# Kernel optimization log

Hardware: AMD Instinct MI355X
Metric: run time of the kernel (lower is better)

Reference implementation:

```python
import jax, jax.numpy as jnp
import numpy as np


def _box_filter(img):
    # img: [B,1,H,W]; 5x5 uniform kernel, padding=4 -> output [B,1,H+4,W+4]
    k = jnp.full((1, 1, 5, 5), 1.0 / 25.0, dtype=img.dtype)
    return jax.lax.conv_general_dilated(
        img, k, window_strides=(1, 1), padding=((4, 4), (4, 4)),
        dimension_numbers=('NCHW', 'OIHW', 'NCHW'))


def setup_inputs() -> dict:
    key = jax.random.key(0)
    k1, k2 = jax.random.split(key)
    x = jax.random.normal(k1, (64, 1, 512, 512), dtype=jnp.float32)
    y = jax.random.normal(k2, (64, 1, 512, 512), dtype=jnp.float32)
    return {"x": x, "y": y}


def reference(x, y):
    diff = _box_filter(x) - _box_filter(y)
    # faithful to torch.mean(torch.sqrt(diff * diff)) (== mean(|diff|))
    return jnp.mean(jnp.sqrt(diff * diff))
```

## Files before the change

### kernel.cpp

```cpp
#include <hip/hip_runtime.h>


#define IMG_W 512
#define IMG_H 512
#define OUT_W 516
#define OUT_H 516
#define R     8
#define SPI   65
#define NT    256
#define WAVES (NT / 64)
#define NSTRIPS (64 * SPI)
#define NBLK  (NSTRIPS / WAVES)
#define NPART 64
#define DEPTH 4

__global__ __launch_bounds__(NT, 3) void box_loss_kernel(
    const float* __restrict__ x, const float* __restrict__ y,
    float* __restrict__ partial)
{
    const int t    = threadIdx.x;
    const int lane = t & 63;
    const int wid  = t >> 6;

    const int bid  = blockIdx.x;
    const int swz  = (bid & 7) * (NBLK / 8) + (bid >> 3);

    const int strip = swz * WAVES + wid;
    const int b  = strip / SPI;
    const int s  = strip - b * SPI;
    const int i0 = s * R;
    const int c0 = lane * 8;

    const float* xb = x + (size_t)b * (IMG_W * IMG_H) + c0;
    const float* yb = y + (size_t)b * (IMG_W * IMG_H) + c0;

    float4 sxa[DEPTH], sxc[DEPTH], sya[DEPTH], syc[DEPTH];

    auto issue = [&](int p, int r) {
        const int rc = min(max(r, 0), IMG_H - 1);
        const float* xr = xb + (size_t)rc * IMG_W;
        const float* yr = yb + (size_t)rc * IMG_W;
        sxa[p] = *(const float4*)(xr);
        sxc[p] = *(const float4*)(xr + 4);
        sya[p] = *(const float4*)(yr);
        syc[p] = *(const float4*)(yr + 4);
    };

    #pragma unroll
    for (int p = 0; p < DEPTH; ++p) issue(p, i0 - 4 + p);

    float ring[5][8];
    float v[8];
    #pragma unroll
    for (int j = 0; j < 8; ++j) { v[j] = 0.f; ring[4][j] = 0.f; }

    float acc = 0.f;

    #pragma unroll
    for (int k = 0; k < R + 4; ++k) {
        const int r = i0 - 4 + k;
        const int p = k % DEPTH;
        const float m = (r >= 0 && r < IMG_H) ? 1.f : 0.f;

        float d[8];
        d[0] = (sxa[p].x - sya[p].x) * m; d[1] = (sxa[p].y - sya[p].y) * m;
        d[2] = (sxa[p].z - sya[p].z) * m; d[3] = (sxa[p].w - sya[p].w) * m;
        d[4] = (sxc[p].x - syc[p].x) * m; d[5] = (sxc[p].y - syc[p].y) * m;
        d[6] = (sxc[p].z - syc[p].z) * m; d[7] = (sxc[p].w - syc[p].w) * m;

        if (k + DEPTH < R + 4) issue(p, r + DEPTH);

        if (k < 4) {
            #pragma unroll
            for (int j = 0; j < 8; ++j) { ring[k][j] = d[j]; v[j] += d[j]; }
        } else {
            const int i = i0 + (k - 4);
            const int slot = k % 5;
            #pragma unroll
            for (int j = 0; j < 8; ++j) {
                v[j] += d[j] - ring[slot][j];
                ring[slot][j] = d[j];
            }

            float h0 = __shfl_up(v[4], 1, 64);
            float h1 = __shfl_up(v[5], 1, 64);
            float h2 = __shfl_up(v[6], 1, 64);
            float h3 = __shfl_up(v[7], 1, 64);
            if (lane == 0) { h0 = 0.f; h1 = 0.f; h2 = 0.f; h3 = 0.f; }

            const float s0 = h0 + h1 + h2 + h3 + v[0];
            const float s1 = s0 + v[1] - h0;
            const float s2 = s1 + v[2] - h1;
            const float s3 = s2 + v[3] - h2;
            const float s4 = s3 + v[4] - h3;
            const float s5 = s4 + v[5] - v[0];
            const float s6 = s5 + v[6] - v[1];
            const float s7 = s6 + v[7] - v[2];

            const float rowmask = (i < OUT_H) ? 1.f : 0.f;
            acc += rowmask * (fabsf(s0) + fabsf(s1) + fabsf(s2) + fabsf(s3)
                            + fabsf(s4) + fabsf(s5) + fabsf(s6) + fabsf(s7));

            const float em = (lane == 63) ? rowmask : 0.f;
            const float e0 = v[4] + v[5] + v[6] + v[7];
            const float e1 = v[5] + v[6] + v[7];
            const float e2 = v[6] + v[7];
            const float e3 = v[7];
            acc += em * (fabsf(e0) + fabsf(e1) + fabsf(e2) + fabsf(e3));
        }
    }

    #pragma unroll
    for (int off = 32; off > 0; off >>= 1)
        acc += __shfl_down(acc, off, 64);
    if (lane == 0)
        atomicAdd(partial + (strip & (NPART - 1)), acc);
}

__global__ void finalize_kernel(const float* __restrict__ partial,
                                float* __restrict__ out)
{
    float s = 0.f;
    #pragma unroll
    for (int k = 0; k < NPART; ++k) s += partial[k];
    out[0] = s * (1.0f / (25.0f * 64.0f * 516.0f * 516.0f));
}

extern "C" void kernel_launch(void* const* d_in, const int* in_sizes, int n_in,
                              void* d_out, int out_size, void* d_ws, size_t ws_size,
                              hipStream_t stream) {
    const float* x = (const float*)d_in[0];
    const float* y = (const float*)d_in[1];
    float* out = (float*)d_out;
    float* ws  = (float*)d_ws;

    hipMemsetAsync(ws, 0, NPART * sizeof(float), stream);

    dim3 grid(NBLK);
    box_loss_kernel<<<grid, NT, 0, stream>>>(x, y, ws);
    finalize_kernel<<<1, 1, 0, stream>>>(ws, out);
}
```

Before: 173.2 us.

## Load rows in sched-barrier-fenced chunks and lengthen strips to nine rows

```diff
diff --git a/kernel.cpp b/kernel.cpp
--- a/kernel.cpp
+++ b/kernel.cpp
@@ -5,16 +5,34 @@
 #define IMG_H 512
 #define OUT_W 516
 #define OUT_H 516
-#define R     8
-#define SPI   65
+#define R     9
+#define SPI   58
 #define NT    256
 #define WAVES (NT / 64)
 #define NSTRIPS (64 * SPI)
 #define NBLK  (NSTRIPS / WAVES)
 #define NPART 64
-#define DEPTH 4
+#define NROWS 13
 
-__global__ __launch_bounds__(NT, 3) void box_loss_kernel(
+typedef float v4f __attribute__((ext_vector_type(4)));
+
+#define LOADCHUNK(base, nr)                                               \
+    __builtin_amdgcn_sched_barrier(0);                                    \
+    _Pragma("unroll")                                                     \
+    for (int q = 0; q < (nr); ++q) {                                      \
+        const int rc = min(max(i0 - 4 + (base) + q, 0), IMG_H - 1);       \
+        const float* xr = xb + (size_t)rc * IMG_W;                        \
+        xa[q] = *(const v4f*)(xr); xc[q] = *(const v4f*)(xr + 4);         \
+    }                                                                     \
+    _Pragma("unroll")                                                     \
+    for (int q = 0; q < (nr); ++q) {                                      \
+        const int rc = min(max(i0 - 4 + (base) + q, 0), IMG_H - 1);       \
+        const float* yr = yb + (size_t)rc * IMG_W;                        \
+        ya[q] = *(const v4f*)(yr); yc[q] = *(const v4f*)(yr + 4);         \
+    }                                                                     \
+    __builtin_amdgcn_sched_barrier(0);
+
+__global__ __launch_bounds__(NT, 2) void box_loss_kernel(
     const float* __restrict__ x, const float* __restrict__ y,
     float* __restrict__ partial)
 {
@@ -34,20 +52,7 @@
     const float* xb = x + (size_t)b * (IMG_W * IMG_H) + c0;
     const float* yb = y + (size_t)b * (IMG_W * IMG_H) + c0;
 
-    float4 sxa[DEPTH], sxc[DEPTH], sya[DEPTH], syc[DEPTH];
-
-    auto issue = [&](int p, int r) {
-        const int rc = min(max(r, 0), IMG_H - 1);
-        const float* xr = xb + (size_t)rc * IMG_W;
-        const float* yr = yb + (size_t)rc * IMG_W;
-        sxa[p] = *(const float4*)(xr);
-        sxc[p] = *(const float4*)(xr + 4);
-        sya[p] = *(const float4*)(yr);
-        syc[p] = *(const float4*)(yr + 4);
-    };
-
-    #pragma unroll
-    for (int p = 0; p < DEPTH; ++p) issue(p, i0 - 4 + p);
+    v4f xa[5], xc[5], ya[5], yc[5];
 
     float ring[5][8];
     float v[8];
@@ -57,18 +62,19 @@
     float acc = 0.f;
 
     #pragma unroll
-    for (int k = 0; k < R + 4; ++k) {
+    for (int k = 0; k < NROWS; ++k) {
+        if (k == 0) { LOADCHUNK(0, 4); }
+        if (k == 4) { LOADCHUNK(4, 4); }
+        if (k == 8) { LOADCHUNK(8, 5); }
+        const int mI = (k < 4) ? k : (k < 8) ? (k - 4) : (k - 8);
         const int r = i0 - 4 + k;
-        const int p = k % DEPTH;
         const float m = (r >= 0 && r < IMG_H) ? 1.f : 0.f;
 
         float d[8];
-        d[0] = (sxa[p].x - sya[p].x) * m; d[1] = (sxa[p].y - sya[p].y) * m;
-        d[2] = (sxa[p].z - sya[p].z) * m; d[3] = (sxa[p].w - sya[p].w) * m;
-        d[4] = (sxc[p].x - syc[p].x) * m; d[5] = (sxc[p].y - syc[p].y) * m;
-        d[6] = (sxc[p].z - syc[p].z) * m; d[7] = (sxc[p].w - syc[p].w) * m;
-
-        if (k + DEPTH < R + 4) issue(p, r + DEPTH);
+        d[0] = (xa[mI].x - ya[mI].x) * m; d[1] = (xa[mI].y - ya[mI].y) * m;
+        d[2] = (xa[mI].z - ya[mI].z) * m; d[3] = (xa[mI].w - ya[mI].w) * m;
+        d[4] = (xc[mI].x - yc[mI].x) * m; d[5] = (xc[mI].y - yc[mI].y) * m;
+        d[6] = (xc[mI].z - yc[mI].z) * m; d[7] = (xc[mI].w - yc[mI].w) * m;
 
         if (k < 4) {
             #pragma unroll
```

Result: faster. 151.5 us (-12.5%).
